# Optimization experiments

Hardware: AMD Instinct MI355X
Metric: run time of the kernel (lower is better)

The kernel has to match this reference:

```python
import jax, jax.numpy as jnp
import numpy as np

B, S, D_IN, D_OUT, H = 4, 2048, 1024, 1024, 16
HD = D_OUT // H


def setup_inputs() -> dict:
    key = jax.random.key(0)
    ks = jax.random.split(key, 6)
    s = 1.0 / np.sqrt(D_IN)
    x = jax.random.normal(ks[0], (B, S, D_IN), dtype=jnp.float32)
    Wq = jax.random.uniform(ks[1], (D_OUT, D_IN), jnp.float32, -s, s)  # torch Linear weight [out,in]
    Wk = jax.random.uniform(ks[2], (D_OUT, D_IN), jnp.float32, -s, s)
    Wv = jax.random.uniform(ks[3], (D_OUT, D_IN), jnp.float32, -s, s)
    so = 1.0 / np.sqrt(D_OUT)
    Wo = jax.random.uniform(ks[4], (D_OUT, D_OUT), jnp.float32, -so, so)
    bo = jax.random.uniform(ks[5], (D_OUT,), jnp.float32, -so, so)
    return {"x": x, "Wq": Wq, "Wk": Wk, "Wv": Wv, "Wo": Wo, "bo": bo}


def reference(x, Wq, Wk, Wv, Wo, bo):
    b, n, _ = x.shape
    # projections (torch Linear: x @ W^T), split heads -> [b, h, n, hd]
    def heads(y):
        return y.reshape(b, n, H, HD).transpose(0, 2, 1, 3)
    q = heads(x @ Wq.T)
    k = heads(x @ Wk.T)
    v = heads(x @ Wv.T)
    scores = jnp.einsum('bhqd,bhkd->bhqk', q, k)
    causal = jnp.triu(jnp.ones((n, n), dtype=bool), k=1)
    scores = jnp.where(causal, -jnp.inf, scores)
    attn = jax.nn.softmax(scores / np.sqrt(HD), axis=-1)  # dropout p=0.0 -> identity
    ctx = jnp.einsum('bhqk,bhkd->bhqd', attn, v)
    ctx = ctx.transpose(0, 2, 1, 3).reshape(b, n, D_OUT)
    return ctx @ Wo.T + bo
```

## Files before the change

### kernel.cpp

```cpp
#include <hip/hip_runtime.h>
#include <hip/hip_bf16.h>
#include <stdint.h>

#define B_N 4
#define SEQ 2048
#define DMODEL 1024
#define NHEAD 16
#define HDIM 64
#define BHEADS (B_N * NHEAD)
#define MROWS (B_N * SEQ)

typedef short bf16x8_t __attribute__((ext_vector_type(8)));
typedef float f32x4_t __attribute__((ext_vector_type(4)));

static __device__ __forceinline__ unsigned short f2bf(float f) {
  __hip_bfloat16 h = __float2bfloat16(f);
  return __builtin_bit_cast(unsigned short, h);
}

#define GLDS16(gp, lp)                                                        \
  __builtin_amdgcn_global_load_lds(                                           \
      (const __attribute__((address_space(1))) unsigned int*)(gp),            \
      (__attribute__((address_space(3))) unsigned int*)(lp), 16, 0, 0)

__global__ void cast_f32_bf16_v4(const float* __restrict__ in,
                                 unsigned short* __restrict__ out, int n4,
                                 float scale) {
  int i = blockIdx.x * blockDim.x + threadIdx.x;
  if (i >= n4) return;
  float4 v = reinterpret_cast<const float4*>(in)[i];
  ushort4 o;
  o.x = f2bf(v.x * scale); o.y = f2bf(v.y * scale);
  o.z = f2bf(v.z * scale); o.w = f2bf(v.w * scale);
  reinterpret_cast<ushort4*>(out)[i] = o;
}

__global__ void cast_weights(const float* __restrict__ Wq,
                             const float* __restrict__ Wk,
                             const float* __restrict__ Wv,
                             const float* __restrict__ Wo,
                             unsigned short* __restrict__ out) {
  int i = blockIdx.x * blockDim.x + threadIdx.x;
  int mat = i >> 18;
  int off = i & 262143;
  const float* src = (mat == 0) ? Wq : (mat == 1) ? Wk : (mat == 2) ? Wv : Wo;
  float scale = (mat == 0) ? 0.125f : 1.0f;
  float4 v = reinterpret_cast<const float4*>(src)[off];
  ushort4 o;
  o.x = f2bf(v.x * scale); o.y = f2bf(v.y * scale);
  o.z = f2bf(v.z * scale); o.w = f2bf(v.w * scale);
  reinterpret_cast<ushort4*>(out)[i] = o;
}

__global__ __launch_bounds__(256, 2)
void gemm_qkv(const unsigned short* __restrict__ A,
              const unsigned short* __restrict__ W,
              unsigned short* __restrict__ Out) {
  __shared__ __align__(16) unsigned short smem[18432];
  unsigned short* As = smem;
  unsigned short* Bs = smem + 4096;

  const int t = threadIdx.x;
  const int lane = t & 63;
  const int w = t >> 6;
  const int quad = lane >> 4;
  const int l16 = lane & 15;
  const int rowBase = blockIdx.x * 128;
  const int colBase = blockIdx.y * 128;
  const int mat = colBase >> 10;
  const int nl = colBase & 1023;
  const int wr = (w >> 1) * 64;
  const int wc = (w & 1) * 64;
  const int K = DMODEL;

  f32x4_t zero4 = {0.f, 0.f, 0.f, 0.f};
  f32x4_t acc[4][4];
#pragma unroll
  for (int i = 0; i < 4; i++)
#pragma unroll
    for (int j = 0; j < 4; j++) acc[i][j] = zero4;

  const int sseg = ((t & 3) ^ ((t >> 3) & 3)) * 8;
  const unsigned short* Ag0 = A + (size_t)(rowBase + (t >> 2)) * K + sseg;
  const unsigned short* Ag1 = A + (size_t)(rowBase + 64 + (t >> 2)) * K + sseg;
  const unsigned short* Bg0 = W + (size_t)(colBase + (t >> 2)) * K + sseg;
  const unsigned short* Bg1 = W + (size_t)(colBase + 64 + (t >> 2)) * K + sseg;
  char* lA0 = (char*)As + t * 16;
  char* lA1 = (char*)As + t * 16 + 4096;
  char* lB0 = (char*)Bs + t * 16;
  char* lB1 = (char*)Bs + t * 16 + 4096;

  const int qsw = (quad ^ ((l16 >> 1) & 3)) * 8;

  for (int k0 = 0; k0 < K; k0 += 32) {
    GLDS16(Ag0 + k0, lA0);
    GLDS16(Ag1 + k0, lA1);
    GLDS16(Bg0 + k0, lB0);
    GLDS16(Bg1 + k0, lB1);
    __syncthreads();

    bf16x8_t af[4], bfr[4];
#pragma unroll
    for (int rt = 0; rt < 4; rt++)
      af[rt] = *(const bf16x8_t*)((const char*)As +
                                  ((wr + rt * 16 + l16) * 32 + qsw) * 2);
#pragma unroll
    for (int ct = 0; ct < 4; ct++)
      bfr[ct] = *(const bf16x8_t*)((const char*)Bs +
                                   ((wc + ct * 16 + l16) * 32 + qsw) * 2);
#pragma unroll
    for (int rt = 0; rt < 4; rt++)
#pragma unroll
      for (int ct = 0; ct < 4; ct++)
        acc[rt][ct] = __builtin_amdgcn_mfma_f32_16x16x32_bf16(
            af[rt], bfr[ct], acc[rt][ct], 0, 0, 0);
    __syncthreads();
  }

  const int hh = (nl + wc) >> 6;
  const int bb = rowBase >> 11;

  if (mat == 2) {
    unsigned short* T = smem + w * 4608;
#pragma unroll
    for (int ct = 0; ct < 4; ct++)
#pragma unroll
      for (int rt = 0; rt < 4; rt++) {
        ushort4 pk;
        pk.x = f2bf(acc[rt][ct][0]);
        pk.y = f2bf(acc[rt][ct][1]);
        pk.z = f2bf(acc[rt][ct][2]);
        pk.w = f2bf(acc[rt][ct][3]);
        *(ushort4*)&T[(ct * 16 + l16) * 72 + rt * 16 + quad * 4] = pk;
      }
    const int srow = (rowBase & (SEQ - 1)) + wr;
    unsigned short* Cq = Out + 2 * (size_t)MROWS * DMODEL;
#pragma unroll
    for (int it = 0; it < 8; it++) {
      int nn = it * 8 + (lane >> 3);
      int sg = lane & 7;
      uint4 d = *(const uint4*)&T[nn * 72 + sg * 8];
      *(uint4*)(Cq + ((size_t)(bb * NHEAD + hh) * HDIM + nn) * SEQ + srow +
                sg * 8) = d;
    }
  } else {
    unsigned short* T = smem + w * 4608;
#pragma unroll
    for (int rt = 0; rt < 4; rt++)
#pragma unroll
      for (int ct = 0; ct < 4; ct++)
#pragma unroll
        for (int r = 0; r < 4; r++)
          T[(rt * 16 + quad * 4 + r) * 72 + ct * 16 + l16] =
              f2bf(acc[rt][ct][r]);
    unsigned short* Cq = Out + (size_t)mat * MROWS * DMODEL;
#pragma unroll
    for (int it = 0; it < 8; it++) {
      int idx = it * 64 + lane;
      int row = idx >> 3, sg = idx & 7, sgx = sg ^ (row & 7);
      uint4 d = *(const uint4*)&T[row * 72 + sgx * 8];
      int m = rowBase + wr + row;
      int s = m & (SEQ - 1), b = m >> 11;
      *(uint4*)(Cq + (((size_t)(b * NHEAD + hh)) * SEQ + s) * HDIM + sgx * 8) = d;
    }
  }
}

__global__ __launch_bounds__(256, 2)
void gemm_out(const unsigned short* __restrict__ A,
              const unsigned short* __restrict__ Bw,
              float* __restrict__ Cf, const float* __restrict__ bias) {
  __shared__ __align__(16) unsigned short smem[8192];
  unsigned short* As = smem;
  unsigned short* Bs = smem + 4096;
  const int t = threadIdx.x;
  const int lane = t & 63;
  const int w = t >> 6;
  const int quad = lane >> 4;
  const int l16 = lane & 15;
  const int rowBase = blockIdx.x * 128;
  const int colBase = blockIdx.y * 128;
  const int wr = (w >> 1) * 64;
  const int wc = (w & 1) * 64;
  const int K = DMODEL, N = DMODEL;

  f32x4_t zero4 = {0.f, 0.f, 0.f, 0.f};
  f32x4_t acc[4][4];
#pragma unroll
  for (int i = 0; i < 4; i++)
#pragma unroll
    for (int j = 0; j < 4; j++) acc[i][j] = zero4;

  const int sseg = ((t & 3) ^ ((t >> 3) & 3)) * 8;
  const unsigned short* Ag0 = A + (size_t)(rowBase + (t >> 2)) * K + sseg;
  const unsigned short* Ag1 = A + (size_t)(rowBase + 64 + (t >> 2)) * K + sseg;
  const unsigned short* Bg0 = Bw + (size_t)(colBase + (t >> 2)) * K + sseg;
  const unsigned short* Bg1 = Bw + (size_t)(colBase + 64 + (t >> 2)) * K + sseg;
  char* lA0 = (char*)As + t * 16;
  char* lA1 = (char*)As + t * 16 + 4096;
  char* lB0 = (char*)Bs + t * 16;
  char* lB1 = (char*)Bs + t * 16 + 4096;
  const int qsw = (quad ^ ((l16 >> 1) & 3)) * 8;

  for (int k0 = 0; k0 < K; k0 += 32) {
    GLDS16(Ag0 + k0, lA0);
    GLDS16(Ag1 + k0, lA1);
    GLDS16(Bg0 + k0, lB0);
    GLDS16(Bg1 + k0, lB1);
    __syncthreads();
    bf16x8_t af[4], bfr[4];
#pragma unroll
    for (int rt = 0; rt < 4; rt++)
      af[rt] = *(const bf16x8_t*)((const char*)As +
                                  ((wr + rt * 16 + l16) * 32 + qsw) * 2);
#pragma unroll
    for (int ct = 0; ct < 4; ct++)
      bfr[ct] = *(const bf16x8_t*)((const char*)Bs +
                                   ((wc + ct * 16 + l16) * 32 + qsw) * 2);
#pragma unroll
    for (int rt = 0; rt < 4; rt++)
#pragma unroll
      for (int ct = 0; ct < 4; ct++)
        acc[rt][ct] = __builtin_amdgcn_mfma_f32_16x16x32_bf16(
            af[rt], bfr[ct], acc[rt][ct], 0, 0, 0);
    __syncthreads();
  }

#pragma unroll
  for (int rt = 0; rt < 4; rt++)
#pragma unroll
    for (int ct = 0; ct < 4; ct++) {
      int n = colBase + wc + ct * 16 + l16;
      float bv = bias[n];
#pragma unroll
      for (int r = 0; r < 4; r++) {
        int m = rowBase + wr + rt * 16 + quad * 4 + r;
        Cf[(size_t)m * N + n] = acc[rt][ct][r] + bv;
      }
    }
}

__global__ __launch_bounds__(256, 2)
void attn_kernel(const unsigned short* __restrict__ Qg_,
                 const unsigned short* __restrict__ Kg_,
                 const unsigned short* __restrict__ Vtg_,
                 unsigned short* __restrict__ ctx) {
  __shared__ __align__(16) unsigned short Ks[2][4096];
  __shared__ __align__(16) unsigned short Vs[2][4096];
  __shared__ __align__(16) unsigned short Ps[4][2048];

  const int t = threadIdx.x;
  const int lane = t & 63, w = t >> 6;
  const int quad = lane >> 4, l16 = lane & 15;
  const int sw = l16 & 7;
  unsigned short* PsW = &Ps[w][0];

  int qtI[2], bhI[2], ntI[2];
  size_t baseI[2];
  {
    int ra = blockIdx.x, rb = 1023 - (int)blockIdx.x;
    qtI[0] = 15 - (ra >> 6); bhI[0] = ra & 63;
    qtI[1] = 15 - (rb >> 6); bhI[1] = rb & 63;
    ntI[0] = 2 * qtI[0] + 2; ntI[1] = 2 * qtI[1] + 2;
    baseI[0] = (size_t)bhI[0] * SEQ * HDIM;
    baseI[1] = (size_t)bhI[1] * SEQ * HDIM;
  }
  const int total = ntI[0] + ntI[1];

  const int r0 = t >> 3;
  const int s0 = ((t & 7) ^ (r0 & 7)) * 8;
  const int r1 = r0 + 32;

  {
    const unsigned short* Kg = Kg_ + baseI[0];
    const unsigned short* Vg = Vtg_ + baseI[0];
    GLDS16(Kg + r0 * HDIM + s0, (char*)&Ks[0][0] + t * 16);
    GLDS16(Kg + r1 * HDIM + s0, (char*)&Ks[0][0] + t * 16 + 4096);
    GLDS16(Vg + (size_t)r0 * SEQ + s0, (char*)&Vs[0][0] + t * 16);
    GLDS16(Vg + (size_t)r1 * SEQ + s0, (char*)&Vs[0][0] + t * 16 + 4096);
  }

  int ii = 0, jt = 0;
  int q0w = qtI[0] * 128 + w * 32;

  bf16x8_t qf[2][2];
#pragma unroll
  for (int q2 = 0; q2 < 2; q2++)
#pragma unroll
    for (int kh = 0; kh < 2; kh++)
      qf[q2][kh] = *(const bf16x8_t*)(Qg_ + baseI[0] +
          (size_t)(q0w + q2 * 16 + l16) * HDIM + kh * 32 + quad * 8);

  float l_[2] = {0.f, 0.f};
  f32x4_t zero4 = {0.f, 0.f, 0.f, 0.f};
  f32x4_t o[2][4];
#pragma unroll
  for (int q2 = 0; q2 < 2; q2++)
#pragma unroll
    for (int dt = 0; dt < 4; dt++) o[q2][dt] = zero4;

  int buf = 0;
  for (int g = 0; g < total; ++g) {
    __syncthreads();
    if (g + 1 < total) {
      int i2 = (g + 1 >= ntI[0]) ? 1 : 0;
      int j2 = (g + 1) - (i2 ? ntI[0] : 0);
      const unsigned short* Kg = Kg_ + baseI[i2] + (size_t)j2 * 64 * HDIM;
      const unsigned short* Vg = Vtg_ + baseI[i2] + j2 * 64;
      char* kd = (char*)&Ks[buf ^ 1][0] + t * 16;
      char* vd = (char*)&Vs[buf ^ 1][0] + t * 16;
      GLDS16(Kg + r0 * HDIM + s0, kd);
      GLDS16(Kg + r1 * HDIM + s0, kd + 4096);
      GLDS16(Vg + (size_t)r0 * SEQ + s0, vd);
      GLDS16(Vg + (size_t)r1 * SEQ + s0, vd + 4096);
    }

    if (jt * 64 <= q0w + 31) {
      const unsigned short* Kb = &Ks[buf][0];
      const unsigned short* Vb = &Vs[buf][0];
      f32x4_t sc[2][4];
#pragma unroll
      for (int q2 = 0; q2 < 2; q2++)
#pragma unroll
        for (int kt = 0; kt < 4; kt++) sc[q2][kt] = zero4;

#pragma unroll
      for (int kt = 0; kt < 4; kt++)
#pragma unroll
        for (int kh = 0; kh < 2; kh++) {
          bf16x8_t kf = *(const bf16x8_t*)((const char*)Kb +
              ((kt * 16 + l16) * 64 + (((kh * 4 + quad) ^ sw) * 8)) * 2);
          sc[0][kt] = __builtin_amdgcn_mfma_f32_16x16x32_bf16(
              kf, qf[0][kh], sc[0][kt], 0, 0, 0);
          sc[1][kt] = __builtin_amdgcn_mfma_f32_16x16x32_bf16(
              kf, qf[1][kh], sc[1][kt], 0, 0, 0);
        }

      if (jt * 64 + 63 > q0w) {
#pragma unroll
        for (int q2 = 0; q2 < 2; q2++) {
          int q = q0w + q2 * 16 + l16;
#pragma unroll
          for (int kt = 0; kt < 4; kt++)
#pragma unroll
            for (int r = 0; r < 4; r++) {
              int key = jt * 64 + kt * 16 + quad * 4 + r;
              if (key > q) sc[q2][kt][r] = -3.0e38f;
            }
        }
      }

#pragma unroll
      for (int q2 = 0; q2 < 2; q2++) {
        float sum = 0.f;
#pragma unroll
        for (int kt = 0; kt < 4; kt++) {
          float p0 = __expf(sc[q2][kt][0]);
          float p1 = __expf(sc[q2][kt][1]);
          float p2 = __expf(sc[q2][kt][2]);
          float p3 = __expf(sc[q2][kt][3]);
          sum += p0 + p1 + p2 + p3;
          ushort4 pk;
          pk.x = f2bf(p0); pk.y = f2bf(p1); pk.z = f2bf(p2); pk.w = f2bf(p3);
          int u = (kt * 4 + quad) ^ ((l16 & 7) << 1);
          *(ushort4*)&PsW[q2 * 1024 + l16 * 64 + u * 4] = pk;
        }
        sum += __shfl_xor(sum, 16, 64);
        sum += __shfl_xor(sum, 32, 64);
        l_[q2] += sum;
      }

      bf16x8_t pf[2][2];
#pragma unroll
      for (int q2 = 0; q2 < 2; q2++)
#pragma unroll
        for (int kc = 0; kc < 2; kc++) {
          int u = (kc * 8 + quad * 2) ^ ((l16 & 7) << 1);
          pf[q2][kc] = *(const bf16x8_t*)&PsW[q2 * 1024 + l16 * 64 + u * 4];
        }
#pragma unroll
      for (int dt = 0; dt < 4; dt++)
#pragma unroll
        for (int kc = 0; kc < 2; kc++) {
          bf16x8_t vfrag = *(const bf16x8_t*)((const char*)Vb +
              ((dt * 16 + l16) * 64 + (((kc * 4 + quad) ^ sw) * 8)) * 2);
          o[0][dt] = __builtin_amdgcn_mfma_f32_16x16x32_bf16(
              vfrag, pf[0][kc], o[0][dt], 0, 0, 0);
          o[1][dt] = __builtin_amdgcn_mfma_f32_16x16x32_bf16(
              vfrag, pf[1][kc], o[1][dt], 0, 0, 0);
        }
    }

    if (jt == ntI[ii] - 1) {
      const int bidx = bhI[ii] >> 4, h = bhI[ii] & 15;
#pragma unroll
      for (int q2 = 0; q2 < 2; q2++) {
        float inv = 1.0f / l_[q2];
#pragma unroll
        for (int dt = 0; dt < 4; dt++) {
          ushort4 pk;
          pk.x = f2bf(o[q2][dt][0] * inv);
          pk.y = f2bf(o[q2][dt][1] * inv);
          pk.z = f2bf(o[q2][dt][2] * inv);
          pk.w = f2bf(o[q2][dt][3] * inv);
          int u = (dt * 4 + quad) ^ ((l16 & 7) << 1);
          *(ushort4*)&PsW[q2 * 1024 + l16 * 64 + u * 4] = pk;
        }
      }
      {
        int qq = lane >> 2, sg = lane & 3;
#pragma unroll
        for (int q2 = 0; q2 < 2; q2++) {
          int ua = (sg * 2) ^ ((qq & 7) << 1);
          int ub = (sg * 2 + 8) ^ ((qq & 7) << 1);
          uint4 da = *(const uint4*)&PsW[q2 * 1024 + qq * 64 + ua * 4];
          uint4 db = *(const uint4*)&PsW[q2 * 1024 + qq * 64 + ub * 4];
          size_t rowoff =
              ((size_t)(bidx * SEQ + q0w + q2 * 16 + qq)) * DMODEL + h * HDIM;
          *(uint4*)(ctx + rowoff + sg * 8) = da;
          *(uint4*)(ctx + rowoff + (sg + 4) * 8) = db;
        }
      }
      if (ii == 0) {
        ii = 1; jt = 0;
        q0w = qtI[1] * 128 + w * 32;
#pragma unroll
        for (int q2 = 0; q2 < 2; q2++)
#pragma unroll
          for (int kh = 0; kh < 2; kh++)
            qf[q2][kh] = *(const bf16x8_t*)(Qg_ + baseI[1] +
                (size_t)(q0w + q2 * 16 + l16) * HDIM + kh * 32 + quad * 8);
        l_[0] = 0.f; l_[1] = 0.f;
#pragma unroll
        for (int q2 = 0; q2 < 2; q2++)
#pragma unroll
          for (int dt = 0; dt < 4; dt++) o[q2][dt] = zero4;
      }
    } else {
      jt++;
    }
    buf ^= 1;
  }
}

extern "C" void kernel_launch(void* const* d_in, const int* in_sizes, int n_in,
                              void* d_out, int out_size, void* d_ws,
                              size_t ws_size, hipStream_t stream) {
  const float* x  = (const float*)d_in[0];
  const float* Wq = (const float*)d_in[1];
  const float* Wk = (const float*)d_in[2];
  const float* Wv = (const float*)d_in[3];
  const float* Wo = (const float*)d_in[4];
  const float* bo = (const float*)d_in[5];
  float* out = (float*)d_out;

  const size_t XE = (size_t)MROWS * DMODEL;
  const size_t WE = (size_t)DMODEL * DMODEL;

  unsigned short* xb   = (unsigned short*)d_ws;
  unsigned short* wqb  = xb + XE;
  unsigned short* wob  = wqb + 3 * WE;
  unsigned short* Qb   = wqb + 4 * WE;
  unsigned short* Kb   = Qb + XE;
  unsigned short* Vtb  = Kb + XE;
  unsigned short* ctxb = xb;

  cast_f32_bf16_v4<<<(int)(XE / 4 + 255) / 256, 256, 0, stream>>>(x, xb,
      (int)(XE / 4), 1.0f);
  cast_weights<<<(int)(4 * WE / 4 + 255) / 256, 256, 0, stream>>>(Wq, Wk, Wv,
      Wo, wqb);

  gemm_qkv<<<dim3(MROWS / 128, 3 * DMODEL / 128), 256, 0, stream>>>(xb, wqb, Qb);

  attn_kernel<<<dim3(512), 256, 0, stream>>>(Qb, Kb, Vtb, ctxb);

  gemm_out<<<dim3(MROWS / 128, DMODEL / 128), 256, 0, stream>>>(ctxb, wob, out, bo);
}
```

Measured before the change: 239.3 us.

## Launch one block per query tile instead of paired tiles in attention

Removes the pairing scheme where each attention block handled a long and a short causal query tile back-to-back, and instead launches 1024 blocks that each handle one tile. Longest tiles are still scheduled first, so the hardware scheduler does the load balancing. Launch bounds are raised to 3 blocks per CU to get more occupancy. This simplifies the loop and the per-iteration index math, but it loses the explicit balance and the carried pipeline across the two tiles, and the higher occupancy target may force register spills.

```diff
diff --git a/kernel.cpp b/kernel.cpp
--- a/kernel.cpp
+++ b/kernel.cpp
@@ -240,7 +240,7 @@
     }
 }
 
-__global__ __launch_bounds__(256, 2)
+__global__ __launch_bounds__(256, 3)
 void attn_kernel(const unsigned short* __restrict__ Qg_,
                  const unsigned short* __restrict__ Kg_,
                  const unsigned short* __restrict__ Vtg_,
@@ -255,40 +255,32 @@
   const int sw = l16 & 7;
   unsigned short* PsW = &Ps[w][0];
 
-  int qtI[2], bhI[2], ntI[2];
-  size_t baseI[2];
-  {
-    int ra = blockIdx.x, rb = 1023 - (int)blockIdx.x;
-    qtI[0] = 15 - (ra >> 6); bhI[0] = ra & 63;
-    qtI[1] = 15 - (rb >> 6); bhI[1] = rb & 63;
-    ntI[0] = 2 * qtI[0] + 2; ntI[1] = 2 * qtI[1] + 2;
-    baseI[0] = (size_t)bhI[0] * SEQ * HDIM;
-    baseI[1] = (size_t)bhI[1] * SEQ * HDIM;
-  }
-  const int total = ntI[0] + ntI[1];
+  const int rank = blockIdx.x;
+  const int qt = 15 - (rank >> 6);
+  const int bh = rank & 63;
+  const int nt = 2 * qt + 2;
+  const size_t base = (size_t)bh * SEQ * HDIM;
 
   const int r0 = t >> 3;
   const int s0 = ((t & 7) ^ (r0 & 7)) * 8;
   const int r1 = r0 + 32;
 
-  {
-    const unsigned short* Kg = Kg_ + baseI[0];
-    const unsigned short* Vg = Vtg_ + baseI[0];
-    GLDS16(Kg + r0 * HDIM + s0, (char*)&Ks[0][0] + t * 16);
-    GLDS16(Kg + r1 * HDIM + s0, (char*)&Ks[0][0] + t * 16 + 4096);
-    GLDS16(Vg + (size_t)r0 * SEQ + s0, (char*)&Vs[0][0] + t * 16);
-    GLDS16(Vg + (size_t)r1 * SEQ + s0, (char*)&Vs[0][0] + t * 16 + 4096);
-  }
-
-  int ii = 0, jt = 0;
-  int q0w = qtI[0] * 128 + w * 32;
+  const unsigned short* Kg = Kg_ + base;
+  const unsigned short* Vg = Vtg_ + base;
+
+  GLDS16(Kg + r0 * HDIM + s0, (char*)&Ks[0][0] + t * 16);
+  GLDS16(Kg + r1 * HDIM + s0, (char*)&Ks[0][0] + t * 16 + 4096);
+  GLDS16(Vg + (size_t)r0 * SEQ + s0, (char*)&Vs[0][0] + t * 16);
+  GLDS16(Vg + (size_t)r1 * SEQ + s0, (char*)&Vs[0][0] + t * 16 + 4096);
+
+  const int q0w = qt * 128 + w * 32;
 
   bf16x8_t qf[2][2];
 #pragma unroll
   for (int q2 = 0; q2 < 2; q2++)
 #pragma unroll
     for (int kh = 0; kh < 2; kh++)
-      qf[q2][kh] = *(const bf16x8_t*)(Qg_ + baseI[0] +
+      qf[q2][kh] = *(const bf16x8_t*)(Qg_ + base +
           (size_t)(q0w + q2 * 16 + l16) * HDIM + kh * 32 + quad * 8);
 
   float l_[2] = {0.f, 0.f};
@@ -300,19 +292,17 @@
     for (int dt = 0; dt < 4; dt++) o[q2][dt] = zero4;
 
   int buf = 0;
-  for (int g = 0; g < total; ++g) {
+  for (int jt = 0; jt < nt; ++jt) {
     __syncthreads();
-    if (g + 1 < total) {
-      int i2 = (g + 1 >= ntI[0]) ? 1 : 0;
-      int j2 = (g + 1) - (i2 ? ntI[0] : 0);
-      const unsigned short* Kg = Kg_ + baseI[i2] + (size_t)j2 * 64 * HDIM;
-      const unsigned short* Vg = Vtg_ + baseI[i2] + j2 * 64;
+    if (jt + 1 < nt) {
+      const unsigned short* Kg2 = Kg + (size_t)(jt + 1) * 64 * HDIM;
+      const unsigned short* Vg2 = Vg + (jt + 1) * 64;
       char* kd = (char*)&Ks[buf ^ 1][0] + t * 16;
       char* vd = (char*)&Vs[buf ^ 1][0] + t * 16;
-      GLDS16(Kg + r0 * HDIM + s0, kd);
-      GLDS16(Kg + r1 * HDIM + s0, kd + 4096);
-      GLDS16(Vg + (size_t)r0 * SEQ + s0, vd);
-      GLDS16(Vg + (size_t)r1 * SEQ + s0, vd + 4096);
+      GLDS16(Kg2 + r0 * HDIM + s0, kd);
+      GLDS16(Kg2 + r1 * HDIM + s0, kd + 4096);
+      GLDS16(Vg2 + (size_t)r0 * SEQ + s0, vd);
+      GLDS16(Vg2 + (size_t)r1 * SEQ + s0, vd + 4096);
     }
 
     if (jt * 64 <= q0w + 31) {
@@ -390,56 +380,37 @@
               vfrag, pf[1][kc], o[1][dt], 0, 0, 0);
         }
     }
-
-    if (jt == ntI[ii] - 1) {
-      const int bidx = bhI[ii] >> 4, h = bhI[ii] & 15;
-#pragma unroll
-      for (int q2 = 0; q2 < 2; q2++) {
-        float inv = 1.0f / l_[q2];
-#pragma unroll
-        for (int dt = 0; dt < 4; dt++) {
-          ushort4 pk;
-          pk.x = f2bf(o[q2][dt][0] * inv);
-          pk.y = f2bf(o[q2][dt][1] * inv);
-          pk.z = f2bf(o[q2][dt][2] * inv);
-          pk.w = f2bf(o[q2][dt][3] * inv);
-          int u = (dt * 4 + quad) ^ ((l16 & 7) << 1);
-          *(ushort4*)&PsW[q2 * 1024 + l16 * 64 + u * 4] = pk;
-        }
-      }
-      {
-        int qq = lane >> 2, sg = lane & 3;
-#pragma unroll
-        for (int q2 = 0; q2 < 2; q2++) {
-          int ua = (sg * 2) ^ ((qq & 7) << 1);
-          int ub = (sg * 2 + 8) ^ ((qq & 7) << 1);
-          uint4 da = *(const uint4*)&PsW[q2 * 1024 + qq * 64 + ua * 4];
-          uint4 db = *(const uint4*)&PsW[q2 * 1024 + qq * 64 + ub * 4];
-          size_t rowoff =
-              ((size_t)(bidx * SEQ + q0w + q2 * 16 + qq)) * DMODEL + h * HDIM;
-          *(uint4*)(ctx + rowoff + sg * 8) = da;
-          *(uint4*)(ctx + rowoff + (sg + 4) * 8) = db;
-        }
-      }
-      if (ii == 0) {
-        ii = 1; jt = 0;
-        q0w = qtI[1] * 128 + w * 32;
-#pragma unroll
-        for (int q2 = 0; q2 < 2; q2++)
-#pragma unroll
-          for (int kh = 0; kh < 2; kh++)
-            qf[q2][kh] = *(const bf16x8_t*)(Qg_ + baseI[1] +
-                (size_t)(q0w + q2 * 16 + l16) * HDIM + kh * 32 + quad * 8);
-        l_[0] = 0.f; l_[1] = 0.f;
-#pragma unroll
-        for (int q2 = 0; q2 < 2; q2++)
-#pragma unroll
-          for (int dt = 0; dt < 4; dt++) o[q2][dt] = zero4;
-      }
-    } else {
-      jt++;
-    }
     buf ^= 1;
+  }
+
+  const int bidx = bh >> 4, h = bh & 15;
+#pragma unroll
+  for (int q2 = 0; q2 < 2; q2++) {
+    float inv = 1.0f / l_[q2];
+#pragma unroll
+    for (int dt = 0; dt < 4; dt++) {
+      ushort4 pk;
+      pk.x = f2bf(o[q2][dt][0] * inv);
+      pk.y = f2bf(o[q2][dt][1] * inv);
+      pk.z = f2bf(o[q2][dt][2] * inv);
+      pk.w = f2bf(o[q2][dt][3] * inv);
+      int u = (dt * 4 + quad) ^ ((l16 & 7) << 1);
+      *(ushort4*)&PsW[q2 * 1024 + l16 * 64 + u * 4] = pk;
+    }
+  }
+  {
+    int qq = lane >> 2, sg = lane & 3;
+#pragma unroll
+    for (int q2 = 0; q2 < 2; q2++) {
+      int ua = (sg * 2) ^ ((qq & 7) << 1);
+      int ub = (sg * 2 + 8) ^ ((qq & 7) << 1);
+      uint4 da = *(const uint4*)&PsW[q2 * 1024 + qq * 64 + ua * 4];
+      uint4 db = *(const uint4*)&PsW[q2 * 1024 + qq * 64 + ub * 4];
+      size_t rowoff =
+          ((size_t)(bidx * SEQ + q0w + q2 * 16 + qq)) * DMODEL + h * HDIM;
+      *(uint4*)(ctx + rowoff + sg * 8) = da;
+      *(uint4*)(ctx + rowoff + (sg + 4) * 8) = db;
+    }
   }
 }
 
@@ -472,7 +443,7 @@
 
   gemm_qkv<<<dim3(MROWS / 128, 3 * DMODEL / 128), 256, 0, stream>>>(xb, wqb, Qb);
 
-  attn_kernel<<<dim3(512), 256, 0, stream>>>(Qb, Kb, Vtb, ctxb);
+  attn_kernel<<<dim3(1024), 256, 0, stream>>>(Qb, Kb, Vtb, ctxb);
 
   gemm_out<<<dim3(MROWS / 128, DMODEL / 128), 256, 0, stream>>>(ctxb, wob, out, bo);
 }
```

Measured after the change: 233.7 us. 1.02x faster.
